# Optimization experiments

Hardware: AMD Instinct MI355X
Metric: run time of the kernel (lower is better)

The kernel has to match this reference:

```python
import jax, jax.numpy as jnp
import numpy as np

FEAT_STRIDE = 8
SCALES = (4.0, 8.0, 16.0)
RATIOS = (0.5, 1.0, 2.0)
A = len(SCALES) * len(RATIOS)          # 9 anchors per location
PRE_NMS = 2048
POST_NMS = 300
NMS_THRESH = 0.7


def _gen_base_anchors():
    # cube anchors at scale*stride, ratio applied to depth; boxes (x1,y1,z1,x2,y2,z2)
    base = float(FEAT_STRIDE)
    ctr = (base - 1.0) / 2.0
    boxes = []
    for r in RATIOS:
        for s in SCALES:
            w = h = base * s
            d = base * s * r
            boxes.append([ctr - 0.5 * (w - 1), ctr - 0.5 * (h - 1), ctr - 0.5 * (d - 1),
                          ctr + 0.5 * (w - 1), ctr + 0.5 * (h - 1), ctr + 0.5 * (d - 1)])
    return jnp.asarray(boxes, jnp.float32)  # [A,6]


def _all_anchors(D, H, W):
    sz = jnp.arange(D, dtype=jnp.float32) * FEAT_STRIDE
    sy = jnp.arange(H, dtype=jnp.float32) * FEAT_STRIDE
    sx = jnp.arange(W, dtype=jnp.float32) * FEAT_STRIDE
    zz, yy, xx = jnp.meshgrid(sz, sy, sx, indexing='ij')  # order (d,h,w) matches score layout
    shifts = jnp.stack([xx, yy, zz, xx, yy, zz], -1).reshape(-1, 6)  # [K,6]
    return (shifts[:, None, :] + _gen_base_anchors()[None]).reshape(-1, 6)  # [K*A,6]


def _apply_deltas(anchors, deltas):
    w = anchors[:, 3] - anchors[:, 0] + 1.0
    h = anchors[:, 4] - anchors[:, 1] + 1.0
    d = anchors[:, 5] - anchors[:, 2] + 1.0
    cx = anchors[:, 0] + 0.5 * w
    cy = anchors[:, 1] + 0.5 * h
    cz = anchors[:, 2] + 0.5 * d
    dx, dy, dz, dw, dh, dd = [deltas[:, i] for i in range(6)]
    pcx = dx * w + cx; pcy = dy * h + cy; pcz = dz * d + cz
    pw = jnp.exp(dw) * w; ph = jnp.exp(dh) * h; pd = jnp.exp(dd) * d
    return jnp.stack([pcx - 0.5 * pw, pcy - 0.5 * ph, pcz - 0.5 * pd,
                      pcx + 0.5 * pw, pcy + 0.5 * ph, pcz + 0.5 * pd], -1)


def _clip_boxes(boxes, iminfo):  # iminfo = [D_im, H_im, W_im]
    lo = jnp.zeros((6,), boxes.dtype)
    hi = jnp.stack([iminfo[2], iminfo[1], iminfo[0], iminfo[2], iminfo[1], iminfo[0]]) - 1.0
    return jnp.clip(boxes, lo[None, :], hi[None, :])


def _pairwise_iou3d(b):  # b: [N,6]
    lo = jnp.maximum(b[:, None, :3], b[None, :, :3])          # [N,N,3]
    hi = jnp.minimum(b[:, None, 3:], b[None, :, 3:])
    inter = jnp.prod(jnp.clip(hi - lo + 1.0, 0.0), axis=-1)   # [N,N]
    vol = jnp.prod(b[:, 3:] - b[:, :3] + 1.0, axis=-1)        # [N]
    return inter / (vol[:, None] + vol[None, :] - inter)


def _nms_keep(iou):
    N = iou.shape[0]
    idx = jnp.arange(N)
    def body(i, keep):
        sup = (iou[i] > NMS_THRESH) & keep[i] & (idx > i)
        return keep & ~sup
    return jax.lax.fori_loop(0, N, body, jnp.ones((N,), bool))


def _propose_one(scores, deltas, anchors, iminfo):
    boxes = _clip_boxes(_apply_deltas(anchors, deltas), iminfo)  # [KA,6]
    _, order = jax.lax.top_k(scores, PRE_NMS)
    b = boxes[order]                                             # [PRE,6], score-sorted desc
    keep = _nms_keep(_pairwise_iou3d(b))
    key = jnp.where(keep, jnp.arange(PRE_NMS), PRE_NMS)
    sel = jnp.argsort(key)[:POST_NMS]                            # first POST_NMS kept, in score order
    valid = (key[sel] < PRE_NMS).astype(b.dtype)
    return b[sel] * valid[:, None]                               # zero-padded rows if < POST_NMS kept


def _forward(base_feat, im_info, W_conv, b_conv, W_cls, b_cls, W_bbox, b_bbox):
    B, C, D, H, W = base_feat.shape
    x = jax.lax.conv_general_dilated(
        base_feat, W_conv, (1, 1, 1), ((1, 1), (1, 1), (1, 1)),
        dimension_numbers=('NCDHW', 'OIDHW', 'NCDHW'))
    x = jax.nn.relu(x + b_conv[None, :, None, None, None])       # [B,512,D,H,W]
    cls = jnp.einsum('bcdhw,oc->bodhw', x, W_cls) + b_cls[None, :, None, None, None]
    prob = jax.nn.softmax(cls.reshape(B, 2, A, D, H, W), axis=1)  # reshape(x,2) + softmax(dim=1)
    fg = prob[:, 1]                                               # [B,A,D,H,W]
    scores = jnp.transpose(fg, (0, 2, 3, 4, 1)).reshape(B, -1)    # [B, K*A], order (d,h,w,a)
    bb = jnp.einsum('bcdhw,oc->bodhw', x, W_bbox) + b_bbox[None, :, None, None, None]
    deltas = jnp.transpose(bb.reshape(B, A, 6, D, H, W), (0, 3, 4, 5, 1, 2)).reshape(B, -1, 6)
    anchors = _all_anchors(D, H, W)
    rois6 = jax.vmap(lambda s, d, im: _propose_one(s, d, anchors, im))(scores, deltas, im_info)
    bidx = jnp.broadcast_to(jnp.arange(B, dtype=rois6.dtype)[:, None, None], (B, POST_NMS, 1))
    return jnp.concatenate([bidx, rois6], -1)                     # [B, POST_NMS, 7]


def setup_inputs() -> dict:
    key = jax.random.key(0)
    ks = jax.random.split(key, 4)
    B, din, D, H, W = 2, 128, 8, 32, 32
    base_feat = jax.random.normal(ks[0], (B, din, D, H, W), jnp.float32)
    im_info = jnp.asarray([[64.0, 256.0, 256.0]] * B, jnp.float32)  # (D_im, H_im, W_im)
    gt_boxes = jnp.zeros((B, 20, 7), jnp.float32)
    num_boxes = jnp.zeros((B,), jnp.int64)
    W_conv = jax.random.normal(ks[1], (512, din, 3, 3, 3), jnp.float32) * 0.02
    b_conv = jnp.zeros((512,), jnp.float32)
    W_cls = jax.random.normal(ks[2], (2 * A, 512), jnp.float32) * 0.01
    b_cls = jnp.zeros((2 * A,), jnp.float32)
    W_bbox = jax.random.normal(ks[3], (6 * A, 512), jnp.float32) * 0.01
    b_bbox = jnp.zeros((6 * A,), jnp.float32)
    return {"base_feat": base_feat, "im_info": im_info, "gt_boxes": gt_boxes,
            "num_boxes": num_boxes, "W_conv": W_conv, "b_conv": b_conv,
            "W_cls": W_cls, "b_cls": b_cls, "W_bbox": W_bbox, "b_bbox": b_bbox}


def reference(base_feat, im_info, gt_boxes, num_boxes, W_conv, b_conv, W_cls, b_cls, W_bbox, b_bbox):
    # Eval-mode RPN forward: losses are 0 in the original; gt_boxes/num_boxes unused.
    rois = _forward(base_feat, im_info, W_conv, b_conv, W_cls, b_cls, W_bbox, b_bbox)
    return rois
```

## Files before the change

kernel.cpp:

```cpp
#include <hip/hip_runtime.h>
#include <stdint.h>

#define BATCH 2
#define CIN 128
#define COUT 512
#define DD 8
#define PSPAT 8192
#define NA 9
#define NANCH 73728
#define PRE 2048
#define POST 300
#define CAP 4096
#define NMS_TH 0.7f

typedef unsigned short u16;
typedef _Float16 f16x8 __attribute__((ext_vector_type(8)));
typedef float f32x16 __attribute__((ext_vector_type(16)));
typedef unsigned int uint32x4 __attribute__((ext_vector_type(4)));

constexpr size_t OFF_WT   = 0;
constexpr size_t OFF_WHT  = 7077888;
constexpr size_t OFF_X    = 7241728;
constexpr size_t OFF_SC   = 40796160;
constexpr size_t OFF_BX   = 41385984;
constexpr size_t OFF_SB   = 44957696;
constexpr size_t OFF_MK   = 45056000;
constexpr size_t OFF_HIST = 16;
constexpr size_t OFF_CAND = 524304;
constexpr size_t OFF_XH   = 46104576;
constexpr size_t OFF_XL   = 50298880;
constexpr size_t WS_NEED_FAST = 54493184;

#define NT_WT   (27 * 128 * 512)
#define NT_WHT  (512 * 80)
__global__ void k_wtrans(const float* __restrict__ Wc, u16* __restrict__ Wg,
                         const float* __restrict__ Wcls, const float* __restrict__ Wbb,
                         float* __restrict__ Wht) {
    int e = blockIdx.x * blockDim.x + threadIdx.x;
    if (e < NT_WT) {
        const int k    = e & 63;
        const int n    = (e >> 6) & 127;
        const int half = (e >> 13) & 1;
        const int rest = e >> 14;
        const int co = (rest / 27) * 128 + n;
        const int ci = half * 64 + k;
        const int tp = rest % 27;
        const float v = Wc[(co * 128 + ci) * 27 + tp] * 1024.f;
        const _Float16 h = (_Float16)v;
        const _Float16 l = (_Float16)(v - (float)h);
        char* rb = (char*)Wg + (((size_t)(rest * 2 + half)) << 15) + n * 256;
        const int hcol = (k >> 3) ^ (n & 15);
        const int lcol = ((k >> 3) | 8) ^ (n & 15);
        const int kb = (k & 7) << 1;
        *(u16*)(rb + (hcol << 4) + kb) = __builtin_bit_cast(unsigned short, h);
        *(u16*)(rb + (lcol << 4) + kb) = __builtin_bit_cast(unsigned short, l);
        return;
    }
    e -= NT_WT;
    if (e >= NT_WHT) return;
    int q = e % 80;
    int c = e / 80;
    int og = q / 10, k = q % 10;
    int o = og * 9 + k;
    float v = 0.f;
    if (k < 9) v = (o < 18) ? Wcls[o * 512 + c] : Wbb[(o - 18) * 512 + c];
    Wht[e] = v;
}

__global__ __launch_bounds__(256) void k_split(const float* __restrict__ in,
                                               u16* __restrict__ xh, u16* __restrict__ xl) {
    __shared__ float t[128][33];
    const int blk = blockIdx.x;
    const int b = blk >> 8, d = (blk >> 5) & 7, h = blk & 31;
    const int tid = threadIdx.x;
    const float* src = in + ((size_t)b << 20) + d * 1024 + h * 32;
    #pragma unroll
    for (int i = 0; i < 16; ++i) {
        const int e = tid + i * 256;
        const int ci = e >> 5, w = e & 31;
        t[ci][w] = src[(size_t)ci * 8192 + w];
    }
    __syncthreads();
    const size_t ob = (size_t)((b * 8 + d) * 32 + h) * 4096;
    #pragma unroll
    for (int i = 0; i < 16; ++i) {
        const int e = tid + i * 256;
        const int w = e >> 7, ci = e & 127;
        const float v = t[ci][w] * 1024.f;
        const _Float16 hh = (_Float16)v;
        const _Float16 ll = (_Float16)(v - (float)hh);
        xh[ob + w * 128 + ci] = __builtin_bit_cast(unsigned short, hh);
        xl[ob + w * 128 + ci] = __builtin_bit_cast(unsigned short, ll);
    }
}

#define MFMA(A, B, C) __builtin_amdgcn_mfma_f32_32x32x16_f16((A), (B), (C), 0, 0, 0)
#define Z16 {0.f,0.f,0.f,0.f,0.f,0.f,0.f,0.f,0.f,0.f,0.f,0.f,0.f,0.f,0.f,0.f}

#define WISSUE(S, BUF) { \
    const int tap_ = t0 + ((S) >> 1); \
    const char* gw_ = WgB + (((size_t)((nt * 27 + tap_) * 2 + ((S) & 1))) << 15) \
                    + (wv << 13) + ln16; \
    char* lb_ = smem + ((BUF) << 15) + (wv << 13); \
    _Pragma("unroll") \
    for (int j_ = 0; j_ < 8; ++j_) \
        __builtin_amdgcn_global_load_lds( \
            (const __attribute__((address_space(1))) void*)(gw_ + (j_ << 10)), \
            (__attribute__((address_space(3))) void*)(lb_ + (j_ << 10)), 16, 0, 0); }

#define KKSTEP(KK, BH0, BL0, BH1, BL1) { \
    const int ch_ = ((((KK) << 1) + cq) ^ rsw) << 4; \
    const int cl_ = (((((KK) << 1) + cq) | 8) ^ rsw) << 4; \
    const char* r0_ = wb_ + (rm0 << 8); \
    const char* r1_ = wb_ + (rm1 << 8); \
    const f16x8 wh0 = *(const f16x8*)(r0_ + ch_); \
    const f16x8 wl0 = *(const f16x8*)(r0_ + cl_); \
    const f16x8 wh1 = *(const f16x8*)(r1_ + ch_); \
    const f16x8 wl1 = *(const f16x8*)(r1_ + cl_); \
    acc00 = MFMA(wh0, BH0, acc00); acc00 = MFMA(wh0, BL0, acc00); acc00 = MFMA(wl0, BH0, acc00); \
    acc01 = MFMA(wh0, BH1, acc01); acc01 = MFMA(wh0, BL1, acc01); acc01 = MFMA(wl0, BH1, acc01); \
    acc10 = MFMA(wh1, BH0, acc10); acc10 = MFMA(wh1, BL0, acc10); acc10 = MFMA(wl1, BH0, acc10); \
    acc11 = MFMA(wh1, BH1, acc11); acc11 = MFMA(wh1, BL1, acc11); acc11 = MFMA(wl1, BH1, acc11); }

#define EPI(ACC, MI, NI) { \
    const int coB_ = co0 + (wm << 6) + ((MI) << 5) + hl4; \
    const int pt_  = p0 + (wn << 6) + ((NI) << 5) + l31; \
    _Pragma("unroll") \
    for (int g_ = 0; g_ < 4; ++g_) { \
        _Pragma("unroll") \
        for (int q_ = 0; q_ < 4; ++q_) { \
            const int co_ = coB_ + (g_ << 3) + q_; \
            const float v_ = ACC[g_ * 4 + q_] * 9.5367431640625e-07f + bconv[co_]; \
            x[((size_t)((b << 9) + co_) << 13) + pt_] = fmaxf(v_, 0.f); \
        } } }

#define FLD(N, KK, BH, BL) { \
    const int h2_ = hb_ + (N); \
    const bool ok_ = okw_ && ((unsigned)h2_ < 32u); \
    const size_t ix_ = sbase_ + ((size_t)((h2_ & 31) << 5) << 7); \
    const f16x8 vh_ = *(const f16x8*)(xh + ix_ + ((KK) << 4)); \
    const f16x8 vl_ = *(const f16x8*)(xl + ix_ + ((KK) << 4)); \
    BH = ok_ ? vh_ : fz8; \
    BL = ok_ ? vl_ : fz8; }

#define ALOADF(S, P) { \
    const int tap_ = t0 + ((S) >> 1); \
    const int kd_ = tap_ / 9, kh_ = (tap_ / 3) % 3, kw_ = tap_ % 3; \
    const int id_ = d0 + kd_ - 1; \
    const int w2_ = l31 + kw_ - 1; \
    const bool okw_ = (unsigned)w2_ < 32u; \
    const int hb_ = h0 + (wn << 1) + kh_ - 1; \
    const int cio_ = (((S) & 1) << 6) + (cq << 3); \
    const size_t sbase_ = (((size_t)((b << 3) + id_)) << 17) + ((w2_ & 31) << 7) + cio_; \
    FLD(0, 0, P##h00, P##l00) FLD(0, 1, P##h01, P##l01) \
    FLD(0, 2, P##h02, P##l02) FLD(0, 3, P##h03, P##l03) \
    FLD(1, 0, P##h10, P##l10) FLD(1, 1, P##h11, P##l11) \
    FLD(1, 2, P##h12, P##l12) FLD(1, 3, P##h13, P##l13) }

#define COMPUTEF(BUF, P) { \
    const char* wb_ = smem + ((BUF) << 15); \
    KKSTEP(0, P##h00, P##l00, P##h10, P##l10) \
    KKSTEP(1, P##h01, P##l01, P##h11, P##l11) \
    KKSTEP(2, P##h02, P##l02, P##h12, P##l12) \
    KKSTEP(3, P##h03, P##l03, P##h13, P##l13) }

#define VMCNT24 asm volatile("s_waitcnt vmcnt(24)" ::: "memory");
#define VMCNT16 asm volatile("s_waitcnt vmcnt(16)" ::: "memory");
#define VMCNT0  asm volatile("s_waitcnt vmcnt(0)"  ::: "memory");
#define SBAR    __builtin_amdgcn_s_barrier();
#define SCHED0  __builtin_amdgcn_sched_barrier(0);

__global__ __launch_bounds__(256, 2) void k_conv_f(const u16* __restrict__ xh,
                                                   const u16* __restrict__ xl,
                                                   const u16* __restrict__ Wg,
                                                   const float* __restrict__ bconv,
                                                   float* __restrict__ x) {
    __shared__ __align__(16) char smem[65536];
    const int tid  = threadIdx.x;
    const int bx   = blockIdx.x;
    const int nt   = blockIdx.y;
    const int b    = blockIdx.z;
    const int p0   = bx << 7;
    const int d0   = bx >> 3;
    const int h0   = (bx & 7) << 2;
    const int co0  = nt << 7;

    const int lane = tid & 63;
    const int wv   = tid >> 6;
    const int wm   = wv & 1;
    const int wn   = wv >> 1;
    const int l31  = lane & 31;
    const int cq   = lane >> 5;
    const int hl4  = cq << 2;
    const int rsw  = l31 & 15;
    const int rm0  = (wm << 6) + l31;
    const int rm1  = rm0 + 32;
    const int ln16 = lane << 4;

    const int t0   = (d0 == 0) ? 9 : 0;
    const int nTap = 27 - (((d0 == 0) || (d0 == 7)) ? 9 : 0);
    const int NS   = nTap * 2;

    const char* WgB = (const char*)Wg;
    const f16x8 fz8 = {(_Float16)0.f, (_Float16)0.f, (_Float16)0.f, (_Float16)0.f,
                       (_Float16)0.f, (_Float16)0.f, (_Float16)0.f, (_Float16)0.f};

    f16x8 Ah00, Al00, Ah01, Al01, Ah02, Al02, Ah03, Al03,
          Ah10, Al10, Ah11, Al11, Ah12, Al12, Ah13, Al13;
    f16x8 Bh00, Bl00, Bh01, Bl01, Bh02, Bl02, Bh03, Bl03,
          Bh10, Bl10, Bh11, Bl11, Bh12, Bl12, Bh13, Bl13;
    f32x16 acc00 = Z16, acc01 = Z16, acc10 = Z16, acc11 = Z16;

    WISSUE(0, 0)
    SCHED0
    ALOADF(0, A)
    VMCNT16
    SBAR

    for (int s = 0; s < NS; s += 2) {
        WISSUE(s + 1, 1)
        SCHED0
        ALOADF(s + 1, B)
        VMCNT24
        SCHED0
        COMPUTEF(0, A)
        VMCNT16
        SBAR
        if (s + 2 < NS) {
            WISSUE(s + 2, 0)
            SCHED0
            ALOADF(s + 2, A)
            VMCNT24
        } else {
            VMCNT0
        }
        SCHED0
        COMPUTEF(1, B)
        if (s + 2 < NS) {
            VMCNT16
            SBAR
        }
    }

    EPI(acc00, 0, 0)
    EPI(acc01, 0, 1)
    EPI(acc10, 1, 0)
    EPI(acc11, 1, 1)
}

#define PK2(YA, YB, UH, UL) { \
    const float sa_ = (YA) * 1024.f, sb_ = (YB) * 1024.f; \
    const _Float16 ha_ = (_Float16)sa_, hb_ = (_Float16)sb_; \
    const _Float16 la_ = (_Float16)(sa_ - (float)ha_); \
    const _Float16 lb_ = (_Float16)(sb_ - (float)hb_); \
    UH = (unsigned)__builtin_bit_cast(unsigned short, ha_) | \
         ((unsigned)__builtin_bit_cast(unsigned short, hb_) << 16); \
    UL = (unsigned)__builtin_bit_cast(unsigned short, la_) | \
         ((unsigned)__builtin_bit_cast(unsigned short, lb_) << 16); }

#define BLDI(N, KK) { \
    const int h2_ = hb_ + (N); \
    const bool ok_ = okw_ && ((unsigned)h2_ < 32u); \
    const float* ap_ = in + (((size_t)(cb0_ + ((KK) << 4))) << 13) + spo_ + (h2_ << 5); \
    y[N][KK][0] = ok_ ? ap_[0]     : 0.f; \
    y[N][KK][1] = ok_ ? ap_[8192]  : 0.f; \
    y[N][KK][2] = ok_ ? ap_[16384] : 0.f; \
    y[N][KK][3] = ok_ ? ap_[24576] : 0.f; \
    y[N][KK][4] = ok_ ? ap_[32768] : 0.f; \
    y[N][KK][5] = ok_ ? ap_[40960] : 0.f; \
    y[N][KK][6] = ok_ ? ap_[49152] : 0.f; \
    y[N][KK][7] = ok_ ? ap_[57344] : 0.f; }

#define ALOADISS(S) { \
    const int tap_ = t0 + ((S) >> 1); \
    const int kd_ = tap_ / 9, kh_ = (tap_ / 3) % 3, kw_ = tap_ % 3; \
    const int id_ = d0 + kd_ - 1; \
    const int w2_ = l31 + kw_ - 1; \
    const bool okw_ = (unsigned)w2_ < 32u; \
    const int hb_ = h0 + (wn << 1) + kh_ - 1; \
    const int cb0_ = b * CIN + (((S) & 1) << 6) + (cq << 3); \
    const long long spo_ = ((long long)id_ << 10) + w2_; \
    BLDI(0, 0) BLDI(0, 1) BLDI(0, 2) BLDI(0, 3) \
    BLDI(1, 0) BLDI(1, 1) BLDI(1, 2) BLDI(1, 3) }

#define CVTFRAG(N, KK, BH, BL) { \
    unsigned uh0_, uh1_, uh2_, uh3_, ul0_, ul1_, ul2_, ul3_; \
    PK2(y[N][KK][0], y[N][KK][1], uh0_, ul0_) \
    PK2(y[N][KK][2], y[N][KK][3], uh1_, ul1_) \
    PK2(y[N][KK][4], y[N][KK][5], uh2_, ul2_) \
    PK2(y[N][KK][6], y[N][KK][7], uh3_, ul3_) \
    { uint32x4 th_ = {uh0_, uh1_, uh2_, uh3_}; BH = __builtin_bit_cast(f16x8, th_); } \
    { uint32x4 tl_ = {ul0_, ul1_, ul2_, ul3_}; BL = __builtin_bit_cast(f16x8, tl_); } }

#define CVTALL() { \
    CVTFRAG(0, 0, bh00, bl00) CVTFRAG(0, 1, bh01, bl01) \
    CVTFRAG(0, 2, bh02, bl02) CVTFRAG(0, 3, bh03, bl03) \
    CVTFRAG(1, 0, bh10, bl10) CVTFRAG(1, 1, bh11, bl11) \
    CVTFRAG(1, 2, bh12, bl12) CVTFRAG(1, 3, bh13, bl13) }

#define COMPUTE(BUF) { \
    const char* wb_ = smem + ((BUF) << 15); \
    KKSTEP(0, bh00, bl00, bh10, bl10) \
    KKSTEP(1, bh01, bl01, bh11, bl11) \
    KKSTEP(2, bh02, bl02, bh12, bl12) \
    KKSTEP(3, bh03, bl03, bh13, bl13) }

__global__ __launch_bounds__(256, 2) void k_conv(const float* __restrict__ in,
                                                 const u16* __restrict__ Wg,
                                                 const float* __restrict__ bconv,
                                                 float* __restrict__ x) {
    __shared__ __align__(16) char smem[65536];
    const int tid  = threadIdx.x;
    const int bx   = blockIdx.x;
    const int nt   = blockIdx.y;
    const int b    = blockIdx.z;
    const int p0   = bx << 7;
    const int d0   = bx >> 3;
    const int h0   = (bx & 7) << 2;
    const int co0  = nt << 7;

    const int lane = tid & 63;
    const int wv   = tid >> 6;
    const int wm   = wv & 1;
    const int wn   = wv >> 1;
    const int l31  = lane & 31;
    const int cq   = lane >> 5;
    const int hl4  = cq << 2;
    const int rsw  = l31 & 15;
    const int rm0  = (wm << 6) + l31;
    const int rm1  = rm0 + 32;
    const int ln16 = lane << 4;

    const int t0   = (d0 == 0) ? 9 : 0;
    const int nTap = 27 - (((d0 == 0) || (d0 == 7)) ? 9 : 0);
    const int NS   = nTap * 2;

    const char* WgB = (const char*)Wg;

    float y[2][4][8];
    f16x8 bh00, bh01, bh02, bh03, bh10, bh11, bh12, bh13;
    f16x8 bl00, bl01, bl02, bl03, bl10, bl11, bl12, bl13;
    f32x16 acc00 = Z16, acc01 = Z16, acc10 = Z16, acc11 = Z16;

    WISSUE(0, 0)
    ALOADISS(0)
    __syncthreads();

    for (int s = 0; s < NS; ++s) {
        if (s + 1 < NS) { WISSUE(s + 1, (s + 1) & 1) }
        CVTALL()
        __builtin_amdgcn_sched_barrier(0);
        if (s + 1 < NS) { ALOADISS(s + 1) }
        __builtin_amdgcn_sched_barrier(0);
        COMPUTE(s & 1)
        __syncthreads();
    }

    EPI(acc00, 0, 0)
    EPI(acc01, 0, 1)
    EPI(acc10, 1, 0)
    EPI(acc11, 1, 1)
}

__global__ __launch_bounds__(256) void k_heads(const float* __restrict__ x,
                                               const float* __restrict__ Wht,
                                               const float* __restrict__ bcls,
                                               const float* __restrict__ bbb,
                                               const float* __restrict__ iminfo,
                                               float* __restrict__ scores,
                                               float* __restrict__ boxes,
                                               unsigned int* __restrict__ hist) {
    __shared__ __align__(16) float smx[4096];
    __shared__ __align__(16) float Whs[2560];
    __shared__ __align__(16) float ex[10240];
    const int tid = threadIdx.x;
    const int p0  = blockIdx.x * 128;
    const int b   = blockIdx.y;
    const int pl  = tid & 31;
    const int og  = tid >> 5;

    float acc[4][9] = {};

    for (int cc = 0; cc < 512; cc += 32) {
        __syncthreads();
        #pragma unroll
        for (int i = 0; i < 4; ++i) {
            int e4 = tid + i * 256;
            int ch = e4 >> 5;
            int pt4 = (e4 & 31) * 4;
            *(float4*)&smx[ch * 128 + pt4] =
                *(const float4*)&x[((size_t)(b * COUT + cc + ch) << 13) + p0 + pt4];
        }
        #pragma unroll
        for (int i = 0; i < 10; ++i) {
            int e = tid + i * 256;
            Whs[e] = Wht[cc * 80 + e];
        }
        __syncthreads();
        for (int kk = 0; kk < 32; ++kk) {
            float4 a4 = *(const float4*)&smx[kk * 128 + pl * 4];
            const float* wp = &Whs[kk * 80 + og * 10];
            float2 w0 = *(const float2*)(wp);
            float2 w1 = *(const float2*)(wp + 2);
            float2 w2 = *(const float2*)(wp + 4);
            float2 w3 = *(const float2*)(wp + 6);
            float  w8 = wp[8];
            float wv[9] = {w0.x, w0.y, w1.x, w1.y, w2.x, w2.y, w3.x, w3.y, w8};
            #pragma unroll
            for (int k = 0; k < 9; ++k) {
                float wk = wv[k];
                acc[0][k] += a4.x * wk;
                acc[1][k] += a4.y * wk;
                acc[2][k] += a4.z * wk;
                acc[3][k] += a4.w * wk;
            }
        }
    }

    __syncthreads();
    #pragma unroll
    for (int pi = 0; pi < 4; ++pi)
        #pragma unroll
        for (int k = 0; k < 9; ++k)
            ex[(pl * 4 + pi) * 80 + og * 10 + k] = acc[pi][k];
    __syncthreads();

    if (tid < 128) {
        const int p = p0 + tid;
        float v[72];
        #pragma unroll
        for (int og2 = 0; og2 < 8; ++og2)
            #pragma unroll
            for (int k = 0; k < 9; ++k)
                v[og2 * 9 + k] = ex[tid * 80 + og2 * 10 + k];

        const float im0 = iminfo[b * 3 + 0], im1 = iminfo[b * 3 + 1], im2 = iminfo[b * 3 + 2];
        const float hix = im2 - 1.f, hiy = im1 - 1.f, hiz = im0 - 1.f;
        const int d = p >> 10, h = (p >> 5) & 31, w = p & 31;
        const float sx = w * 8.f, sy = h * 8.f, sz = d * 8.f;

        #pragma unroll 1
        for (int a = 0; a < 9; ++a) {
            float c0 = v[a] + bcls[a];
            float c1 = v[9 + a] + bcls[9 + a];
            float m  = fmaxf(c0, c1);
            float e0 = expf(c0 - m), e1 = expf(c1 - m);
            float sc = e1 / (e0 + e1);
            scores[b * NANCH + p * 9 + a] = sc;
            atomicAdd(&hist[b * 65536 + (__float_as_uint(sc) >> 16)], 1u);

            float aw = (float)(32 << (a % 3));
            float ad = aw * 0.5f * (float)(1 << (a / 3));
            float ax1 = sx + 3.5f - 0.5f * (aw - 1.f);
            float ax2 = sx + 3.5f + 0.5f * (aw - 1.f);
            float ay1 = sy + 3.5f - 0.5f * (aw - 1.f);
            float ay2 = sy + 3.5f + 0.5f * (aw - 1.f);
            float az1 = sz + 3.5f - 0.5f * (ad - 1.f);
            float az2 = sz + 3.5f + 0.5f * (ad - 1.f);
            float ww_ = ax2 - ax1 + 1.f, hh_ = ay2 - ay1 + 1.f, dd_ = az2 - az1 + 1.f;
            float cx = ax1 + 0.5f * ww_, cy = ay1 + 0.5f * hh_, cz = az1 + 0.5f * dd_;

            const float* dv = &v[18 + a * 6];
            float dx = dv[0] + bbb[a * 6 + 0];
            float dy = dv[1] + bbb[a * 6 + 1];
            float dz = dv[2] + bbb[a * 6 + 2];
            float dw = dv[3] + bbb[a * 6 + 3];
            float dh = dv[4] + bbb[a * 6 + 4];
            float dd2 = dv[5] + bbb[a * 6 + 5];
            float pcx = dx * ww_ + cx, pcy = dy * hh_ + cy, pcz = dz * dd_ + cz;
            float pw = expf(dw) * ww_, ph = expf(dh) * hh_, pd = expf(dd2) * dd_;
            float x1 = fminf(fmaxf(pcx - 0.5f * pw, 0.f), hix);
            float y1 = fminf(fmaxf(pcy - 0.5f * ph, 0.f), hiy);
            float z1 = fminf(fmaxf(pcz - 0.5f * pd, 0.f), hiz);
            float x2 = fminf(fmaxf(pcx + 0.5f * pw, 0.f), hix);
            float y2 = fminf(fmaxf(pcy + 0.5f * ph, 0.f), hiy);
            float z2 = fminf(fmaxf(pcz + 0.5f * pd, 0.f), hiz);
            float* bp = &boxes[(size_t)(b * NANCH + p * 9 + a) * 6];
            bp[0] = x1; bp[1] = y1; bp[2] = z1; bp[3] = x2; bp[4] = y2; bp[5] = z2;
        }
    }
}

__global__ __launch_bounds__(1024) void k_cutcompact(const float* __restrict__ scores,
                                                     const unsigned int* __restrict__ hist,
                                                     unsigned long long* __restrict__ cand) {
    __shared__ unsigned int cs[1024], scan[1024];
    __shared__ unsigned int sh_cut, sh_pos;
    const int b = blockIdx.x, tid = threadIdx.x;
    const unsigned int* h = hist + b * 65536;
    unsigned int s = 0;
    for (int i = 0; i < 64; ++i) s += h[tid * 64 + i];
    cs[tid] = s; scan[tid] = s;
    if (tid == 0) sh_pos = 0;
    __syncthreads();
    for (int d = 1; d < 1024; d <<= 1) {
        unsigned int v = scan[tid];
        unsigned int add = (tid + d < 1024) ? scan[tid + d] : 0u;
        __syncthreads();
        scan[tid] = v + add;
        __syncthreads();
    }
    unsigned int above = (tid + 1 < 1024) ? scan[tid + 1] : 0u;
    if (above < PRE && above + cs[tid] >= PRE) {
        unsigned int cum = above;
        for (int x = tid * 64 + 63; x >= tid * 64; --x) {
            cum += h[x];
            if (cum >= PRE) { sh_cut = (unsigned int)x; break; }
        }
    }
    __syncthreads();
    const unsigned int cut = sh_cut;
    const float* sc = scores + b * NANCH;
    for (int i = tid; i < NANCH; i += 1024) {
        unsigned int u = __float_as_uint(sc[i]);
        if ((u >> 16) >= cut) {
            unsigned int pos = atomicAdd(&sh_pos, 1u);
            if (pos < CAP) cand[b * CAP + pos] = ((unsigned long long)(~u) << 32) | (unsigned)i;
        }
    }
    __syncthreads();
    const unsigned int cnt = (sh_pos < CAP) ? sh_pos : CAP;
    for (int i = (int)cnt + tid; i < CAP; i += 1024)
        cand[b * CAP + i] = ~0ull;
}

__global__ __launch_bounds__(1024) void k_sort2(const unsigned long long* __restrict__ cand,
                                                const float* __restrict__ boxes,
                                                float* __restrict__ sboxes) {
    __shared__ unsigned long long sk[CAP];
    const int b = blockIdx.x, tid = threadIdx.x;
    for (int i = tid; i < CAP; i += 1024) sk[i] = cand[b * CAP + i];
    __syncthreads();
    for (int k = 2; k <= CAP; k <<= 1) {
        for (int j = k >> 1; j > 0; j >>= 1) {
            #pragma unroll 1
            for (int i = tid; i < CAP; i += 1024) {
                int ixj = i ^ j;
                if (ixj > i) {
                    unsigned long long va = sk[i], vb = sk[ixj];
                    bool up = ((i & k) == 0);
                    if ((va > vb) == up) { sk[i] = vb; sk[ixj] = va; }
                }
            }
            __syncthreads();
        }
    }
    for (int r = tid; r < PRE; r += 1024) {
        unsigned int n = (unsigned int)(sk[r] & 0xFFFFFFFFull);
        const float* src = &boxes[(size_t)(b * NANCH + (int)n) * 6];
        float* dst = &sboxes[(size_t)(b * PRE + r) * 6];
        #pragma unroll
        for (int c = 0; c < 6; ++c) dst[c] = src[c];
    }
}

__global__ __launch_bounds__(256) void k_mask(const float* __restrict__ sboxes,
                                              unsigned long long* __restrict__ mask) {
    if (blockIdx.y < blockIdx.x) return;
    __shared__ float rb[64 * 6], cb[64 * 6];
    const int i0 = blockIdx.x * 64, j0 = blockIdx.y * 64, b = blockIdx.z;
    const int tid = threadIdx.x;
    for (int e = tid; e < 384; e += 256) {
        rb[e] = sboxes[(size_t)(b * PRE + i0) * 6 + e];
        cb[e] = sboxes[(size_t)(b * PRE + j0) * 6 + e];
    }
    __syncthreads();
    const int wave = tid >> 6, lane = tid & 63;
    const float bx1 = cb[lane * 6 + 0], by1 = cb[lane * 6 + 1], bz1 = cb[lane * 6 + 2];
    const float bx2 = cb[lane * 6 + 3], by2 = cb[lane * 6 + 4], bz2 = cb[lane * 6 + 5];
    const float vb = (bx2 - bx1 + 1.f) * (by2 - by1 + 1.f) * (bz2 - bz1 + 1.f);
    const int j = j0 + lane;
    for (int rr = 0; rr < 16; ++rr) {
        const int il = wave * 16 + rr;
        const int i = i0 + il;
        float ax1 = rb[il * 6 + 0], ay1 = rb[il * 6 + 1], az1 = rb[il * 6 + 2];
        float ax2 = rb[il * 6 + 3], ay2 = rb[il * 6 + 4], az2 = rb[il * 6 + 5];
        float va = (ax2 - ax1 + 1.f) * (ay2 - ay1 + 1.f) * (az2 - az1 + 1.f);
        float ix = fmaxf(fminf(ax2, bx2) - fmaxf(ax1, bx1) + 1.f, 0.f);
        float iy = fmaxf(fminf(ay2, by2) - fmaxf(ay1, by1) + 1.f, 0.f);
        float iz = fmaxf(fminf(az2, bz2) - fmaxf(az1, bz1) + 1.f, 0.f);
        float inter = ix * iy * iz;
        float iou = inter / (va + vb - inter);
        bool bit = (j > i) && (iou > NMS_TH);
        unsigned long long word = __ballot(bit);
        if (lane == 0) mask[(size_t)(b * PRE + i) * 32 + (j0 >> 6)] = word;
    }
}

__global__ __launch_bounds__(64) void k_nms(const unsigned long long* __restrict__ mask,
                                            const float* __restrict__ sboxes,
                                            float* __restrict__ out) {
    const int b = blockIdx.x, lane = threadIdx.x;
    __shared__ int sel[POST];
    unsigned long long keep = ~0ull;
    const int lw = lane & 31;
    const unsigned long long* mrow = mask + (size_t)b * PRE * 32 + lw;
    unsigned long long b0 = mrow[0 * 32], b1 = mrow[1 * 32], b2 = mrow[2 * 32], b3 = mrow[3 * 32];
    unsigned long long b4 = mrow[4 * 32], b5 = mrow[5 * 32], b6 = mrow[6 * 32], b7 = mrow[7 * 32];
    int kcount = 0;

#define NMS_STEP(J, BUF)                                                        \
    {                                                                           \
        int i = i0 + (J);                                                       \
        unsigned long long cur = (lw >= (i >> 6)) ? BUF : 0ull;                 \
        int nr = i0 + 8 + (J);                                                  \
        BUF = (nr < PRE) ? mrow[(size_t)nr * 32] : 0ull;                        \
        unsigned long long kw = __shfl(keep, i >> 6);                           \
        if ((kw >> (i & 63)) & 1ull) {                                          \
            if (lane < 32) keep &= ~cur;                                        \
            if (lane == 0 && kcount < POST) sel[kcount] = i;                    \
            ++kcount;                                                           \
            if (kcount >= POST) goto nms_done;                                  \
        }                                                                       \
    }

    for (int i0 = 0; i0 < PRE; i0 += 8) {
        NMS_STEP(0, b0) NMS_STEP(1, b1) NMS_STEP(2, b2) NMS_STEP(3, b3)
        NMS_STEP(4, b4) NMS_STEP(5, b5) NMS_STEP(6, b6) NMS_STEP(7, b7)
    }
nms_done:
    __syncthreads();
    const int kc = kcount;
    for (int r = lane; r < POST; r += 64) {
        float* op = &out[(size_t)(b * POST + r) * 7];
        op[0] = (float)b;
        if (r < kc) {
            const float* sb = &sboxes[(size_t)(b * PRE + sel[r]) * 6];
            #pragma unroll
            for (int c = 0; c < 6; ++c) op[1 + c] = sb[c];
        } else {
            #pragma unroll
            for (int c = 0; c < 6; ++c) op[1 + c] = 0.f;
        }
    }
#undef NMS_STEP
}

extern "C" void kernel_launch(void* const* d_in, const int* in_sizes, int n_in,
                              void* d_out, int out_size, void* d_ws, size_t ws_size,
                              hipStream_t stream) {
    const float* base_feat = (const float*)d_in[0];
    const float* im_info   = (const float*)d_in[1];
    const float* W_conv    = (const float*)d_in[4];
    const float* b_conv    = (const float*)d_in[5];
    const float* W_cls     = (const float*)d_in[6];
    const float* b_cls     = (const float*)d_in[7];
    const float* W_bbox    = (const float*)d_in[8];
    const float* b_bbox    = (const float*)d_in[9];

    char* ws = (char*)d_ws;
    u16* Wg        = (u16*)(ws + OFF_WT);
    float* Wht     = (float*)(ws + OFF_WHT);
    float* x       = (float*)(ws + OFF_X);
    float* scores  = (float*)(ws + OFF_SC);
    float* boxes   = (float*)(ws + OFF_BX);
    float* sboxes  = (float*)(ws + OFF_SB);
    unsigned long long* mask = (unsigned long long*)(ws + OFF_MK);
    unsigned int* hist = (unsigned int*)(ws + OFF_HIST);
    unsigned long long* cand = (unsigned long long*)(ws + OFF_CAND);
    u16* xh        = (u16*)(ws + OFF_XH);
    u16* xl        = (u16*)(ws + OFF_XL);

    const int NTRANS = NT_WT + NT_WHT;
    k_wtrans<<<(NTRANS + 255) / 256, 256, 0, stream>>>(W_conv, Wg, W_cls, W_bbox, Wht);
    if (ws_size >= WS_NEED_FAST) {
        k_split<<<512, 256, 0, stream>>>(base_feat, xh, xl);
        k_conv_f<<<dim3(64, 4, 2), 256, 0, stream>>>(xh, xl, Wg, b_conv, x);
    } else {
        k_conv<<<dim3(64, 4, 2), 256, 0, stream>>>(base_feat, Wg, b_conv, x);
    }
    hipMemsetAsync(hist, 0, BATCH * 65536 * sizeof(unsigned int), stream);
    k_heads<<<dim3(64, 2), 256, 0, stream>>>(x, Wht, b_cls, b_bbox, im_info, scores, boxes, hist);
    k_cutcompact<<<BATCH, 1024, 0, stream>>>(scores, hist, cand);
    k_sort2<<<BATCH, 1024, 0, stream>>>(cand, boxes, sboxes);
    k_mask<<<dim3(32, 32, 2), 256, 0, stream>>>(sboxes, mask);
    k_nms<<<BATCH, 64, 0, stream>>>(mask, sboxes, (float*)d_out);
}
```

Measured before the change: 642.2 us.

## Store split fp16 input in channel-octet-major layout and interleave MFMA chains

The fp16 hi/lo split of the input is now stored as [h][oct][w][8] instead of [h][w][ci], so each thread writes packed 16-byte vectors and the conv's per-lane B-operand loads change addressing to match. The MFMA sequence in each k-step is reordered so four independent accumulators alternate instead of three dependent MFMAs issuing back to back on one accumulator. Together these aim to cut uncoalesced 2-byte stores and MFMA dependency stalls. The new layout alters the global access pattern of the conv's activation loads, which may coalesce differently.

```diff
diff --git a/kernel.cpp b/kernel.cpp
--- a/kernel.cpp
+++ b/kernel.cpp
@@ -83,14 +83,26 @@
     __syncthreads();
     const size_t ob = (size_t)((b * 8 + d) * 32 + h) * 4096;
     #pragma unroll
-    for (int i = 0; i < 16; ++i) {
+    for (int i = 0; i < 2; ++i) {
         const int e = tid + i * 256;
-        const int w = e >> 7, ci = e & 127;
-        const float v = t[ci][w] * 1024.f;
-        const _Float16 hh = (_Float16)v;
-        const _Float16 ll = (_Float16)(v - (float)hh);
-        xh[ob + w * 128 + ci] = __builtin_bit_cast(unsigned short, hh);
-        xl[ob + w * 128 + ci] = __builtin_bit_cast(unsigned short, ll);
+        const int oct = e >> 5, w = e & 31;
+        unsigned sh0, sh1, sh2, sh3, sl0, sl1, sl2, sl3;
+        #define SPL2(C, SH, SL) { \
+            const float va_ = t[oct * 8 + 2*(C)][w] * 1024.f; \
+            const float vb_ = t[oct * 8 + 2*(C)+1][w] * 1024.f; \
+            const _Float16 ha_ = (_Float16)va_, hb_ = (_Float16)vb_; \
+            const _Float16 la_ = (_Float16)(va_ - (float)ha_); \
+            const _Float16 lb_ = (_Float16)(vb_ - (float)hb_); \
+            SH = (unsigned)__builtin_bit_cast(unsigned short, ha_) | \
+                 ((unsigned)__builtin_bit_cast(unsigned short, hb_) << 16); \
+            SL = (unsigned)__builtin_bit_cast(unsigned short, la_) | \
+                 ((unsigned)__builtin_bit_cast(unsigned short, lb_) << 16); }
+        SPL2(0, sh0, sl0) SPL2(1, sh1, sl1) SPL2(2, sh2, sl2) SPL2(3, sh3, sl3)
+        #undef SPL2
+        uint32x4 vh = {sh0, sh1, sh2, sh3};
+        uint32x4 vl = {sl0, sl1, sl2, sl3};
+        *(uint32x4*)(xh + ob + (size_t)e * 8) = vh;
+        *(uint32x4*)(xl + ob + (size_t)e * 8) = vl;
     }
 }
 
@@ -117,10 +129,18 @@
     const f16x8 wl0 = *(const f16x8*)(r0_ + cl_); \
     const f16x8 wh1 = *(const f16x8*)(r1_ + ch_); \
     const f16x8 wl1 = *(const f16x8*)(r1_ + cl_); \
-    acc00 = MFMA(wh0, BH0, acc00); acc00 = MFMA(wh0, BL0, acc00); acc00 = MFMA(wl0, BH0, acc00); \
-    acc01 = MFMA(wh0, BH1, acc01); acc01 = MFMA(wh0, BL1, acc01); acc01 = MFMA(wl0, BH1, acc01); \
-    acc10 = MFMA(wh1, BH0, acc10); acc10 = MFMA(wh1, BL0, acc10); acc10 = MFMA(wl1, BH0, acc10); \
-    acc11 = MFMA(wh1, BH1, acc11); acc11 = MFMA(wh1, BL1, acc11); acc11 = MFMA(wl1, BH1, acc11); }
+    acc00 = MFMA(wh0, BH0, acc00); \
+    acc01 = MFMA(wh0, BH1, acc01); \
+    acc10 = MFMA(wh1, BH0, acc10); \
+    acc11 = MFMA(wh1, BH1, acc11); \
+    acc00 = MFMA(wh0, BL0, acc00); \
+    acc01 = MFMA(wh0, BL1, acc01); \
+    acc10 = MFMA(wh1, BL0, acc10); \
+    acc11 = MFMA(wh1, BL1, acc11); \
+    acc00 = MFMA(wl0, BH0, acc00); \
+    acc01 = MFMA(wl0, BH1, acc01); \
+    acc10 = MFMA(wl1, BH0, acc10); \
+    acc11 = MFMA(wl1, BH1, acc11); }
 
 #define EPI(ACC, MI, NI) { \
     const int coB_ = co0 + (wm << 6) + ((MI) << 5) + hl4; \
@@ -137,9 +157,9 @@
 #define FLD(N, KK, BH, BL) { \
     const int h2_ = hb_ + (N); \
     const bool ok_ = okw_ && ((unsigned)h2_ < 32u); \
-    const size_t ix_ = sbase_ + ((size_t)((h2_ & 31) << 5) << 7); \
-    const f16x8 vh_ = *(const f16x8*)(xh + ix_ + ((KK) << 4)); \
-    const f16x8 vl_ = *(const f16x8*)(xl + ix_ + ((KK) << 4)); \
+    const size_t ix_ = sbase_ + ((size_t)(h2_ & 31) << 12); \
+    const f16x8 vh_ = *(const f16x8*)(xh + ix_ + ((KK) << 9)); \
+    const f16x8 vl_ = *(const f16x8*)(xl + ix_ + ((KK) << 9)); \
     BH = ok_ ? vh_ : fz8; \
     BL = ok_ ? vl_ : fz8; }
 
@@ -150,8 +170,8 @@
     const int w2_ = l31 + kw_ - 1; \
     const bool okw_ = (unsigned)w2_ < 32u; \
     const int hb_ = h0 + (wn << 1) + kh_ - 1; \
-    const int cio_ = (((S) & 1) << 6) + (cq << 3); \
-    const size_t sbase_ = (((size_t)((b << 3) + id_)) << 17) + ((w2_ & 31) << 7) + cio_; \
+    const int oc0_ = (((S) & 1) << 3) + cq; \
+    const size_t sbase_ = (((size_t)((b << 3) + id_)) << 17) + (oc0_ << 8) + ((w2_ & 31) << 3); \
     FLD(0, 0, P##h00, P##l00) FLD(0, 1, P##h01, P##l01) \
     FLD(0, 2, P##h02, P##l02) FLD(0, 3, P##h03, P##l03) \
     FLD(1, 0, P##h10, P##l10) FLD(1, 1, P##h11, P##l11) \
```

New measurement: 557.1 us. 13.2% less time.
